# Performance work log

Hardware: AMD Instinct MI355X
Metric: run time of the kernel (lower is better)

## Reference

```python
import jax, jax.numpy as jnp
import numpy as np

B, N, DIM = 8, 16384, 256
DIM_HEAD, NUM_HEADS = 64, 8
D = DIM_HEAD * NUM_HEADS  # 512
SCALE = DIM_HEAD ** (-0.5)


def setup_inputs() -> dict:
    key = jax.random.key(0)
    ks = jax.random.split(key, 11)
    s = 0.02
    return {
        "x": jax.random.normal(ks[0], (B, N, DIM), dtype=jnp.float32),
        "Wq": jax.random.normal(ks[1], (DIM, D), dtype=jnp.float32) * s,
        "bq": jax.random.normal(ks[2], (D,), dtype=jnp.float32) * s,
        "Wk": jax.random.normal(ks[3], (DIM, D), dtype=jnp.float32) * s,
        "bk": jax.random.normal(ks[4], (D,), dtype=jnp.float32) * s,
        "qw": jax.random.normal(ks[5], (D, 1), dtype=jnp.float32),  # query_weight parameter
        "Wp": jax.random.normal(ks[6], (D, D), dtype=jnp.float32) * s,
        "bp": jax.random.normal(ks[7], (D,), dtype=jnp.float32) * s,
        "Wo": jax.random.normal(ks[8], (D, DIM_HEAD), dtype=jnp.float32) * s,
        "bo": jax.random.normal(ks[9], (DIM_HEAD,), dtype=jnp.float32) * s,
    }


def reference(x, Wq, bq, Wk, bk, qw, Wp, bp, Wo, bo):
    # query, key: [B, N, D]
    query = jnp.einsum("bnc,cd->bnd", x, Wq) + bq
    key = jnp.einsum("bnc,cd->bnd", x, Wk) + bk
    # per-token scalar score: [B, N, 1]
    score = (query @ qw) * SCALE
    # global attention context: sum over sequence axis -> [B, 1, D]
    attn_weight = jnp.sum(score * query, axis=1, keepdims=True)
    # broadcast (repeat over N), gate keys, project, residual add of query
    out = jnp.einsum("bnd,de->bne", attn_weight * key, Wp) + bp + query
    # output projection D -> dim_head: [B, N, DIM_HEAD]
    out = jnp.einsum("bnd,dh->bnh", out, Wo) + bo
    return out
```

## Files before the change

### kernel.cpp

```cpp
#include <hip/hip_runtime.h>
#include <hip/hip_bf16.h>


#define NN 16384
#define CC 256
#define DD 512
#define HH 64
#define SCALE_F 0.125f

#define OFF_SX    0
#define OFF_TSUM  2048
#define OFF_WQQ   2056
#define OFF_BQQ   2312
#define OFF_WPWO  2320
#define OFF_WQWO  35088
#define OFF_CBIAS 51472
#define OFF_BEFF  51536
#define OFF_WEFFT 52048

typedef unsigned short ushort_t;
typedef __attribute__((ext_vector_type(8))) short short8;
typedef __attribute__((ext_vector_type(4))) float floatx4;

__device__ __forceinline__ unsigned short f2bf(float f) {
    __hip_bfloat16 h = __float2bfloat16(f);
    return __builtin_bit_cast(unsigned short, h);
}

__global__ __launch_bounds__(256) void k_prep(
    const float* __restrict__ Wq, const float* __restrict__ bq,
    const float* __restrict__ qw, const float* __restrict__ Wp,
    const float* __restrict__ bp, const float* __restrict__ Wo,
    const float* __restrict__ bo, float* __restrict__ ws)
{
    __shared__ float lds[4096];
    const int tid = threadIdx.x;
    const int bid = blockIdx.x;

    if (bid < 64) {
        const int d0 = bid * 8;
        for (int i = tid; i < 4096; i += 256) lds[i] = Wp[d0 * 512 + i];
        __syncthreads();
        for (int o = tid; o < 512; o += 256) {
            const int dl = o >> 6, h = o & 63;
            float acc = 0.f;
            for (int e = 0; e < 512; ++e) acc += lds[dl * 512 + e] * Wo[e * 64 + h];
            ws[OFF_WPWO + (d0 + dl) * 64 + h] = acc;
        }
    } else if (bid == 64) {
        for (int i = tid; i < 512; i += 256) lds[i] = qw[i];
        __syncthreads();
        {
            const float* wr = Wq + tid * 512;
            float acc = 0.f;
            for (int d = 0; d < 512; ++d) acc += wr[d] * lds[d];
            ws[OFF_WQQ + tid] = acc;
        }
        if (tid == 0) {
            float s = 0.f;
            for (int d = 0; d < 512; ++d) s += bq[d] * lds[d];
            ws[OFF_BQQ] = s;
        }
        for (int i = tid; i < 2056; i += 256) ws[OFF_SX + i] = 0.f;
    } else if (bid == 65) {
        if (tid < 64) {
            float acc = bo[tid];
            for (int d = 0; d < 512; ++d) acc += (bq[d] + bp[d]) * Wo[d * 64 + tid];
            ws[OFF_CBIAS + tid] = acc;
        }
    } else {
        const int c0 = (bid - 66) * 8;
        for (int i = tid; i < 4096; i += 256) lds[i] = Wq[c0 * 512 + i];
        __syncthreads();
        for (int o = tid; o < 512; o += 256) {
            const int cl = o >> 6, h = o & 63;
            float acc = 0.f;
            for (int d = 0; d < 512; ++d) acc += lds[cl * 512 + d] * Wo[d * 64 + h];
            ws[OFF_WQWO + (c0 + cl) * 64 + h] = acc;
        }
    }
}

__global__ __launch_bounds__(256) void k_phase1(
    const float* __restrict__ x, float* __restrict__ ws)
{
    const int b = blockIdx.y;
    const int tid = threadIdx.x;
    const int lane = tid & 63;
    const int wave = tid >> 6;

    __shared__ float lacc[256];
    __shared__ float ltsum;
    lacc[tid] = 0.f;
    if (tid == 0) ltsum = 0.f;
    const floatx4 wv = *(const floatx4*)(ws + OFF_WQQ + lane * 4);
    const float bqq = ws[OFF_BQQ];
    __syncthreads();

    const int row0 = blockIdx.x * 128 + wave * 32;
    const float* xb = x + (size_t)b * NN * CC;

    float a0 = 0.f, a1 = 0.f, a2 = 0.f, a3 = 0.f, ts = 0.f;
    for (int i = 0; i < 32; ++i) {
        const floatx4 xv = *(const floatx4*)(xb + (size_t)(row0 + i) * CC + lane * 4);
        float p = xv[0] * wv[0] + xv[1] * wv[1] + xv[2] * wv[2] + xv[3] * wv[3];
        p += __shfl_xor(p, 32);
        p += __shfl_xor(p, 16);
        p += __shfl_xor(p, 8);
        p += __shfl_xor(p, 4);
        p += __shfl_xor(p, 2);
        p += __shfl_xor(p, 1);
        const float t = SCALE_F * (p + bqq);
        a0 += t * xv[0]; a1 += t * xv[1]; a2 += t * xv[2]; a3 += t * xv[3];
        ts += t;
    }
    atomicAdd(&lacc[lane * 4 + 0], a0);
    atomicAdd(&lacc[lane * 4 + 1], a1);
    atomicAdd(&lacc[lane * 4 + 2], a2);
    atomicAdd(&lacc[lane * 4 + 3], a3);
    if (lane == 0) atomicAdd(&ltsum, ts);
    __syncthreads();
    atomicAdd(&ws[OFF_SX + b * 256 + tid], lacc[tid]);
    if (tid == 0) atomicAdd(&ws[OFF_TSUM + b], ltsum);
}

__global__ __launch_bounds__(256) void k_weff(
    const float* __restrict__ Wq, const float* __restrict__ bq,
    const float* __restrict__ Wk, const float* __restrict__ bk,
    float* __restrict__ ws)
{
    const int b = blockIdx.y;
    const int c0 = blockIdx.x * 32;
    const int tid = threadIdx.x;

    __shared__ float lsx[256];
    __shared__ float law[512];
    __shared__ float lts;
    __shared__ float wpT[128 * 64];
    lsx[tid] = ws[OFF_SX + b * 256 + tid];
    if (tid == 0) lts = ws[OFF_TSUM + b];
    __syncthreads();
    const float tsum = lts;

    for (int d = tid; d < 512; d += 256) {
        float acc = tsum * bq[d];
        for (int c = 0; c < 256; ++c) acc += lsx[c] * Wq[c * 512 + d];
        law[d] = acc;
    }
    __syncthreads();

    const int c = c0 + (tid >> 3);
    const int hb = (tid & 7) * 8;
    float acc[8];
#pragma unroll
    for (int j = 0; j < 8; ++j) acc[j] = ws[OFF_WQWO + c * 64 + hb + j];

    for (int t4 = 0; t4 < 4; ++t4) {
        const int d0 = t4 * 128;
        for (int i = tid; i < 8192; i += 256) wpT[i] = ws[OFF_WPWO + d0 * 64 + i];
        __syncthreads();
        for (int dl = 0; dl < 128; ++dl) {
            const float g = Wk[c * 512 + d0 + dl] * law[d0 + dl];
            const floatx4 p0 = *(const floatx4*)(wpT + dl * 64 + hb);
            const floatx4 p1 = *(const floatx4*)(wpT + dl * 64 + hb + 4);
            acc[0] += g * p0[0]; acc[1] += g * p0[1];
            acc[2] += g * p0[2]; acc[3] += g * p0[3];
            acc[4] += g * p1[0]; acc[5] += g * p1[1];
            acc[6] += g * p1[2]; acc[7] += g * p1[3];
        }
        __syncthreads();
    }

    ushort_t* wt = (ushort_t*)(ws + OFF_WEFFT) + (size_t)b * (HH * CC);
#pragma unroll
    for (int j = 0; j < 8; ++j)
        wt[(size_t)(hb + j) * CC + c] = f2bf(acc[j]);

    if (blockIdx.x == 0 && tid < 64) {
        float a = ws[OFF_CBIAS + tid];
        for (int d = 0; d < 512; ++d)
            a += bk[d] * law[d] * ws[OFF_WPWO + d * 64 + tid];
        ws[OFF_BEFF + b * 64 + tid] = a;
    }
}

__global__ __launch_bounds__(256) void k_out(
    const float* __restrict__ x, const float* __restrict__ ws,
    float* __restrict__ out)
{
    const int b = blockIdx.y;
    const int tid = threadIdx.x;
    const int lane = tid & 63;
    const int wave = tid >> 6;
    const int quad = lane >> 4;
    const int l15 = lane & 15;
    const int row0 = blockIdx.x * 64 + wave * 16;

    __shared__ __align__(16) ushort_t lwt[64 * 264];
    const ushort_t* wt = (const ushort_t*)(ws + OFF_WEFFT) + (size_t)b * (HH * CC);
    for (int o = tid; o < 2048; o += 256) {
        const int h = o >> 5, seg = o & 31;
        *(short8*)(lwt + h * 264 + seg * 8) = *(const short8*)(wt + h * 256 + seg * 8);
    }

    const float* xr = x + ((size_t)b * NN + row0 + l15) * CC + quad * 8;
    short8 afrag[8];
#pragma unroll
    for (int kk = 0; kk < 8; ++kk) {
        const floatx4 u0 = *(const floatx4*)(xr + kk * 32);
        const floatx4 u1 = *(const floatx4*)(xr + kk * 32 + 4);
        short8 t;
        t[0] = (short)f2bf(u0[0]); t[1] = (short)f2bf(u0[1]);
        t[2] = (short)f2bf(u0[2]); t[3] = (short)f2bf(u0[3]);
        t[4] = (short)f2bf(u1[0]); t[5] = (short)f2bf(u1[1]);
        t[6] = (short)f2bf(u1[2]); t[7] = (short)f2bf(u1[3]);
        afrag[kk] = t;
    }
    __syncthreads();

    floatx4 acc[4];
#pragma unroll
    for (int ht = 0; ht < 4; ++ht)
#pragma unroll
        for (int r = 0; r < 4; ++r) acc[ht][r] = 0.f;

#pragma unroll
    for (int kk = 0; kk < 8; ++kk)
#pragma unroll
        for (int ht = 0; ht < 4; ++ht) {
            const short8 bf =
                *(const short8*)(lwt + (ht * 16 + l15) * 264 + quad * 8 + kk * 32);
            acc[ht] = __builtin_amdgcn_mfma_f32_16x16x32_bf16(
                afrag[kk], bf, acc[ht], 0, 0, 0);
        }

    const float* beff = ws + OFF_BEFF + b * 64;
#pragma unroll
    for (int ht = 0; ht < 4; ++ht) {
        const int h = ht * 16 + l15;
        const float bias = beff[h];
#pragma unroll
        for (int r = 0; r < 4; ++r) {
            const int row = row0 + quad * 4 + r;
            out[((size_t)b * NN + row) * HH + h] = acc[ht][r] + bias;
        }
    }
}

extern "C" void kernel_launch(void* const* d_in, const int* in_sizes, int n_in,
                              void* d_out, int out_size, void* d_ws, size_t ws_size,
                              hipStream_t stream) {
    const float* x  = (const float*)d_in[0];
    const float* Wq = (const float*)d_in[1];
    const float* bq = (const float*)d_in[2];
    const float* Wk = (const float*)d_in[3];
    const float* bk = (const float*)d_in[4];
    const float* qw = (const float*)d_in[5];
    const float* Wp = (const float*)d_in[6];
    const float* bp = (const float*)d_in[7];
    const float* Wo = (const float*)d_in[8];
    const float* bo = (const float*)d_in[9];
    float* ws = (float*)d_ws;
    float* out = (float*)d_out;

    hipLaunchKernelGGL(k_prep,   dim3(98),      dim3(256), 0, stream,
                       Wq, bq, qw, Wp, bp, Wo, bo, ws);
    hipLaunchKernelGGL(k_phase1, dim3(128, 8),  dim3(256), 0, stream, x, ws);
    hipLaunchKernelGGL(k_weff,   dim3(8, 8),    dim3(256), 0, stream,
                       Wq, bq, Wk, bk, ws);
    hipLaunchKernelGGL(k_out,    dim3(256, 8),  dim3(256), 0, stream, x, ws, out);
}
```

Before: 328.1 us.

## Fuse four kernels into one cooperative persistent kernel with grid syncs

Merges the prep, reduction, weight-fold and output kernels into a single cooperative launch of 1024 blocks, separated by grid-wide barriers, and falls back to four launches if the cooperative launch fails. The aim is to cut the launch gaps between small dependent kernels. It also reworks the phase-1 reduction so each lane holds 16 floats and reduces over fewer shuffles, and has each output block process two row tiles so the bf16 weight tile staged in LDS is reused. The risks are grid.sync overhead, lower occupancy from launch_bounds(256,4), and phase C running on only 64 blocks while the rest of the grid waits.

New measurement: 1.201 ms. 3.66x slower.

```diff
diff --git a/kernel.cpp b/kernel.cpp
--- a/kernel.cpp
+++ b/kernel.cpp
@@ -1,5 +1,6 @@
 #include <hip/hip_runtime.h>
 #include <hip/hip_bf16.h>
+#include <hip/hip_cooperative_groups.h>
 
 
 #define NN 16384
@@ -7,6 +8,8 @@
 #define DD 512
 #define HH 64
 #define SCALE_F 0.125f
+#define GRID_BLKS 1024
+#define SMEM_BYTES 33792
 
 #define OFF_SX    0
 #define OFF_TSUM  2048
@@ -27,224 +30,328 @@
     return __builtin_bit_cast(unsigned short, h);
 }
 
-__global__ __launch_bounds__(256) void k_prep(
+__device__ __forceinline__ void phaseA(
+    const float* __restrict__ Wq, const float* __restrict__ bq,
+    const float* __restrict__ qw, const float* __restrict__ Wp,
+    const float* __restrict__ bp, const float* __restrict__ Wo,
+    const float* __restrict__ bo, float* __restrict__ ws,
+    unsigned char* smem)
+{
+    const int tid = threadIdx.x;
+    for (int vb = blockIdx.x; vb < 195; vb += gridDim.x) {
+        if (vb < 128) {
+            float* lds = (float*)smem;
+            const int d0 = vb * 4;
+            for (int i = tid; i < 2048; i += 256) lds[i] = Wp[d0 * 512 + i];
+            __syncthreads();
+            const int dl = tid >> 6, h = tid & 63;
+            float acc = 0.f;
+            for (int e = 0; e < 512; ++e)
+                acc = fmaf(lds[dl * 512 + e], Wo[e * 64 + h], acc);
+            ws[OFF_WPWO + (d0 + dl) * 64 + h] = acc;
+        } else if (vb < 192) {
+            float* lds = (float*)smem;
+            const int c0 = (vb - 128) * 4;
+            for (int i = tid; i < 2048; i += 256) lds[i] = Wq[c0 * 512 + i];
+            __syncthreads();
+            const int cl = tid >> 6, h = tid & 63;
+            float acc = 0.f;
+            for (int e = 0; e < 512; ++e)
+                acc = fmaf(lds[cl * 512 + e], Wo[e * 64 + h], acc);
+            ws[OFF_WQWO + (c0 + cl) * 64 + h] = acc;
+        } else if (vb == 192) {
+            float* lds = (float*)smem;
+            float* lb  = (float*)(smem + 2048);
+            for (int i = tid; i < 512; i += 256) lds[i] = qw[i];
+            if (tid == 0) *lb = 0.f;
+            __syncthreads();
+            const float* wr = Wq + tid * 512;
+            float acc = 0.f;
+            for (int d = 0; d < 512; ++d) acc = fmaf(wr[d], lds[d], acc);
+            ws[OFF_WQQ + tid] = acc;
+            float pb = fmaf(bq[tid], lds[tid], bq[tid + 256] * lds[tid + 256]);
+#pragma unroll
+            for (int m = 1; m < 64; m <<= 1) pb += __shfl_xor(pb, m);
+            if ((tid & 63) == 0) atomicAdd(lb, pb);
+            __syncthreads();
+            if (tid == 0) ws[OFF_BQQ] = *lb;
+        } else if (vb == 193) {
+            if (tid < 64) {
+                float acc = bo[tid];
+                for (int d = 0; d < 512; ++d)
+                    acc = fmaf(bq[d] + bp[d], Wo[d * 64 + tid], acc);
+                ws[OFF_CBIAS + tid] = acc;
+            }
+        } else {
+            for (int i = tid; i < 2056; i += 256) ws[OFF_SX + i] = 0.f;
+        }
+        __syncthreads();
+    }
+}
+
+__device__ __forceinline__ void phaseB(
+    const float* __restrict__ x, float* __restrict__ ws, unsigned char* smem)
+{
+    const int tid  = threadIdx.x;
+    const int lane = tid & 63;
+    const int wave = tid >> 6;
+    const int quad = lane >> 4;
+    const int l15  = lane & 15;
+    float* lacc  = (float*)smem;
+    float* ltsum = (float*)(smem + 1024);
+
+    floatx4 wv[4];
+#pragma unroll
+    for (int j = 0; j < 4; ++j)
+        wv[j] = *(const floatx4*)(ws + OFF_WQQ + j * 64 + l15 * 4);
+    const float bqq = ws[OFF_BQQ];
+
+    for (int vb = blockIdx.x; vb < 1024; vb += gridDim.x) {
+        const int b = vb >> 7;
+        const int rbase = (vb & 127) * 128;
+        lacc[tid] = 0.f;
+        if (tid == 0) *ltsum = 0.f;
+        __syncthreads();
+
+        const float* xb = x + (size_t)b * NN * CC;
+        const int r0 = rbase + wave * 32 + quad;
+        floatx4 accs[4];
+#pragma unroll
+        for (int j = 0; j < 4; ++j)
+#pragma unroll
+            for (int k = 0; k < 4; ++k) accs[j][k] = 0.f;
+        float ts = 0.f;
+
+#pragma unroll 2
+        for (int it = 0; it < 8; ++it) {
+            const float* xr = xb + (size_t)(r0 + it * 4) * CC + l15 * 4;
+            const floatx4 x0 = *(const floatx4*)(xr);
+            const floatx4 x1 = *(const floatx4*)(xr + 64);
+            const floatx4 x2 = *(const floatx4*)(xr + 128);
+            const floatx4 x3 = *(const floatx4*)(xr + 192);
+            float p = 0.f;
+#pragma unroll
+            for (int k = 0; k < 4; ++k) {
+                p = fmaf(x0[k], wv[0][k], p);
+                p = fmaf(x1[k], wv[1][k], p);
+                p = fmaf(x2[k], wv[2][k], p);
+                p = fmaf(x3[k], wv[3][k], p);
+            }
+            p += __shfl_xor(p, 1);
+            p += __shfl_xor(p, 2);
+            p += __shfl_xor(p, 4);
+            p += __shfl_xor(p, 8);
+            const float t = SCALE_F * (p + bqq);
+            ts += t;
+#pragma unroll
+            for (int k = 0; k < 4; ++k) {
+                accs[0][k] = fmaf(t, x0[k], accs[0][k]);
+                accs[1][k] = fmaf(t, x1[k], accs[1][k]);
+                accs[2][k] = fmaf(t, x2[k], accs[2][k]);
+                accs[3][k] = fmaf(t, x3[k], accs[3][k]);
+            }
+        }
+
+#pragma unroll
+        for (int j = 0; j < 4; ++j)
+#pragma unroll
+            for (int k = 0; k < 4; ++k) {
+                float v = accs[j][k];
+                v += __shfl_xor(v, 16);
+                v += __shfl_xor(v, 32);
+                if (quad == 0) atomicAdd(&lacc[j * 64 + l15 * 4 + k], v);
+            }
+        if (l15 == 0) atomicAdd(ltsum, ts);
+        __syncthreads();
+        atomicAdd(&ws[OFF_SX + b * 256 + tid], lacc[tid]);
+        if (tid == 0) atomicAdd(&ws[OFF_TSUM + b], *ltsum);
+        __syncthreads();
+    }
+}
+
+__device__ __forceinline__ void phaseC(
+    const float* __restrict__ Wq, const float* __restrict__ bq,
+    const float* __restrict__ Wk, const float* __restrict__ bk,
+    float* __restrict__ ws, unsigned char* smem)
+{
+    const int tid = threadIdx.x;
+    for (int vb = blockIdx.x; vb < 64; vb += gridDim.x) {
+        const int b = vb >> 3;
+        const int c0 = (vb & 7) * 32;
+        float* lsx = (float*)smem;
+        float* law = (float*)(smem + 1024);
+        float* lts = (float*)(smem + 3072);
+        float* wpT = (float*)(smem + 3088);
+
+        lsx[tid] = ws[OFF_SX + b * 256 + tid];
+        if (tid == 0) *lts = ws[OFF_TSUM + b];
+        __syncthreads();
+        const float tsum = *lts;
+
+        for (int d = tid; d < 512; d += 256) {
+            float acc = tsum * bq[d];
+            for (int c = 0; c < 256; ++c) acc = fmaf(lsx[c], Wq[c * 512 + d], acc);
+            law[d] = acc;
+        }
+        __syncthreads();
+
+        const int c = c0 + (tid >> 3);
+        const int hb = (tid & 7) * 8;
+        float acc[8];
+#pragma unroll
+        for (int j = 0; j < 8; ++j) acc[j] = ws[OFF_WQWO + c * 64 + hb + j];
+
+        for (int t8 = 0; t8 < 8; ++t8) {
+            const int d0 = t8 * 64;
+            for (int i = tid; i < 4096; i += 256) wpT[i] = ws[OFF_WPWO + d0 * 64 + i];
+            __syncthreads();
+            for (int dl = 0; dl < 64; ++dl) {
+                const float g = Wk[c * 512 + d0 + dl] * law[d0 + dl];
+                const floatx4 p0 = *(const floatx4*)(wpT + dl * 64 + hb);
+                const floatx4 p1 = *(const floatx4*)(wpT + dl * 64 + hb + 4);
+                acc[0] = fmaf(g, p0[0], acc[0]); acc[1] = fmaf(g, p0[1], acc[1]);
+                acc[2] = fmaf(g, p0[2], acc[2]); acc[3] = fmaf(g, p0[3], acc[3]);
+                acc[4] = fmaf(g, p1[0], acc[4]); acc[5] = fmaf(g, p1[1], acc[5]);
+                acc[6] = fmaf(g, p1[2], acc[6]); acc[7] = fmaf(g, p1[3], acc[7]);
+            }
+            __syncthreads();
+        }
+
+        ushort_t* wt = (ushort_t*)(ws + OFF_WEFFT) + (size_t)b * (HH * CC);
+#pragma unroll
+        for (int j = 0; j < 8; ++j)
+            wt[(size_t)(hb + j) * CC + c] = f2bf(acc[j]);
+
+        if ((vb & 7) == 0 && tid < 64) {
+            float a = ws[OFF_CBIAS + tid];
+            for (int d = 0; d < 512; ++d)
+                a = fmaf(bk[d] * law[d], ws[OFF_WPWO + d * 64 + tid], a);
+            ws[OFF_BEFF + b * 64 + tid] = a;
+        }
+        __syncthreads();
+    }
+}
+
+__device__ __forceinline__ void phaseD(
+    const float* __restrict__ x, const float* __restrict__ ws,
+    float* __restrict__ out, unsigned char* smem)
+{
+    const int tid  = threadIdx.x;
+    const int lane = tid & 63;
+    const int wave = tid >> 6;
+    const int quad = lane >> 4;
+    const int l15  = lane & 15;
+    ushort_t* lwt = (ushort_t*)smem;
+
+    for (int vb = blockIdx.x; vb < 1024; vb += gridDim.x) {
+        const int b = vb >> 7;
+        const int rt0 = vb & 127;
+        const ushort_t* wt = (const ushort_t*)(ws + OFF_WEFFT) + (size_t)b * (HH * CC);
+        for (int o = tid; o < 2048; o += 256) {
+            const int h = o >> 5, seg = o & 31;
+            *(short8*)(lwt + h * 264 + seg * 8) = *(const short8*)(wt + h * 256 + seg * 8);
+        }
+        __syncthreads();
+
+        const float* beff = ws + OFF_BEFF + b * 64;
+        float bias[4];
+#pragma unroll
+        for (int ht = 0; ht < 4; ++ht) bias[ht] = beff[ht * 16 + l15];
+
+#pragma unroll
+        for (int s = 0; s < 2; ++s) {
+            const int row0 = (rt0 + s * 128) * 64 + wave * 16;
+            const float* xr = x + ((size_t)b * NN + row0 + l15) * CC + quad * 8;
+            short8 afrag[8];
+#pragma unroll
+            for (int kk = 0; kk < 8; ++kk) {
+                const floatx4 u0 = *(const floatx4*)(xr + kk * 32);
+                const floatx4 u1 = *(const floatx4*)(xr + kk * 32 + 4);
+                short8 t;
+                t[0] = (short)f2bf(u0[0]); t[1] = (short)f2bf(u0[1]);
+                t[2] = (short)f2bf(u0[2]); t[3] = (short)f2bf(u0[3]);
+                t[4] = (short)f2bf(u1[0]); t[5] = (short)f2bf(u1[1]);
+                t[6] = (short)f2bf(u1[2]); t[7] = (short)f2bf(u1[3]);
+                afrag[kk] = t;
+            }
+            floatx4 acc[4];
+#pragma unroll
+            for (int ht = 0; ht < 4; ++ht)
+#pragma unroll
+                for (int r = 0; r < 4; ++r) acc[ht][r] = 0.f;
+
+#pragma unroll
+            for (int kk = 0; kk < 8; ++kk)
+#pragma unroll
+                for (int ht = 0; ht < 4; ++ht) {
+                    const short8 bf =
+                        *(const short8*)(lwt + (ht * 16 + l15) * 264 + quad * 8 + kk * 32);
+                    acc[ht] = __builtin_amdgcn_mfma_f32_16x16x32_bf16(
+                        afrag[kk], bf, acc[ht], 0, 0, 0);
+                }
+
+#pragma unroll
+            for (int ht = 0; ht < 4; ++ht) {
+                const int h = ht * 16 + l15;
+#pragma unroll
+                for (int r = 0; r < 4; ++r) {
+                    const int row = row0 + quad * 4 + r;
+                    out[((size_t)b * NN + row) * HH + h] = acc[ht][r] + bias[ht];
+                }
+            }
+        }
+        __syncthreads();
+    }
+}
+
+__global__ __launch_bounds__(256, 4) void k_fused(
+    const float* __restrict__ x,  const float* __restrict__ Wq,
+    const float* __restrict__ bq, const float* __restrict__ Wk,
+    const float* __restrict__ bk, const float* __restrict__ qw,
+    const float* __restrict__ Wp, const float* __restrict__ bp,
+    const float* __restrict__ Wo, const float* __restrict__ bo,
+    float* __restrict__ ws, float* __restrict__ out)
+{
+    __shared__ __align__(16) unsigned char smem[SMEM_BYTES];
+    cooperative_groups::grid_group grid = cooperative_groups::this_grid();
+    phaseA(Wq, bq, qw, Wp, bp, Wo, bo, ws, smem);
+    grid.sync();
+    phaseB(x, ws, smem);
+    grid.sync();
+    phaseC(Wq, bq, Wk, bk, ws, smem);
+    grid.sync();
+    phaseD(x, ws, out, smem);
+}
+
+__global__ __launch_bounds__(256, 4) void k_phA(
     const float* __restrict__ Wq, const float* __restrict__ bq,
     const float* __restrict__ qw, const float* __restrict__ Wp,
     const float* __restrict__ bp, const float* __restrict__ Wo,
     const float* __restrict__ bo, float* __restrict__ ws)
 {
-    __shared__ float lds[4096];
-    const int tid = threadIdx.x;
-    const int bid = blockIdx.x;
-
-    if (bid < 64) {
-        const int d0 = bid * 8;
-        for (int i = tid; i < 4096; i += 256) lds[i] = Wp[d0 * 512 + i];
-        __syncthreads();
-        for (int o = tid; o < 512; o += 256) {
-            const int dl = o >> 6, h = o & 63;
-            float acc = 0.f;
-            for (int e = 0; e < 512; ++e) acc += lds[dl * 512 + e] * Wo[e * 64 + h];
-            ws[OFF_WPWO + (d0 + dl) * 64 + h] = acc;
-        }
-    } else if (bid == 64) {
-        for (int i = tid; i < 512; i += 256) lds[i] = qw[i];
-        __syncthreads();
-        {
-            const float* wr = Wq + tid * 512;
-            float acc = 0.f;
-            for (int d = 0; d < 512; ++d) acc += wr[d] * lds[d];
-            ws[OFF_WQQ + tid] = acc;
-        }
-        if (tid == 0) {
-            float s = 0.f;
-            for (int d = 0; d < 512; ++d) s += bq[d] * lds[d];
-            ws[OFF_BQQ] = s;
-        }
-        for (int i = tid; i < 2056; i += 256) ws[OFF_SX + i] = 0.f;
-    } else if (bid == 65) {
-        if (tid < 64) {
-            float acc = bo[tid];
-            for (int d = 0; d < 512; ++d) acc += (bq[d] + bp[d]) * Wo[d * 64 + tid];
-            ws[OFF_CBIAS + tid] = acc;
-        }
-    } else {
-        const int c0 = (bid - 66) * 8;
-        for (int i = tid; i < 4096; i += 256) lds[i] = Wq[c0 * 512 + i];
-        __syncthreads();
-        for (int o = tid; o < 512; o += 256) {
-            const int cl = o >> 6, h = o & 63;
-            float acc = 0.f;
-            for (int d = 0; d < 512; ++d) acc += lds[cl * 512 + d] * Wo[d * 64 + h];
-            ws[OFF_WQWO + (c0 + cl) * 64 + h] = acc;
-        }
-    }
-}
-
-__global__ __launch_bounds__(256) void k_phase1(
+    __shared__ __align__(16) unsigned char smem[SMEM_BYTES];
+    phaseA(Wq, bq, qw, Wp, bp, Wo, bo, ws, smem);
+}
+__global__ __launch_bounds__(256, 4) void k_phB(
     const float* __restrict__ x, float* __restrict__ ws)
 {
-    const int b = blockIdx.y;
-    const int tid = threadIdx.x;
-    const int lane = tid & 63;
-    const int wave = tid >> 6;
-
-    __shared__ float lacc[256];
-    __shared__ float ltsum;
-    lacc[tid] = 0.f;
-    if (tid == 0) ltsum = 0.f;
-    const floatx4 wv = *(const floatx4*)(ws + OFF_WQQ + lane * 4);
-    const float bqq = ws[OFF_BQQ];
-    __syncthreads();
-
-    const int row0 = blockIdx.x * 128 + wave * 32;
-    const float* xb = x + (size_t)b * NN * CC;
-
-    float a0 = 0.f, a1 = 0.f, a2 = 0.f, a3 = 0.f, ts = 0.f;
-    for (int i = 0; i < 32; ++i) {
-        const floatx4 xv = *(const floatx4*)(xb + (size_t)(row0 + i) * CC + lane * 4);
-        float p = xv[0] * wv[0] + xv[1] * wv[1] + xv[2] * wv[2] + xv[3] * wv[3];
-        p += __shfl_xor(p, 32);
-        p += __shfl_xor(p, 16);
-        p += __shfl_xor(p, 8);
-        p += __shfl_xor(p, 4);
-        p += __shfl_xor(p, 2);
-        p += __shfl_xor(p, 1);
-        const float t = SCALE_F * (p + bqq);
-        a0 += t * xv[0]; a1 += t * xv[1]; a2 += t * xv[2]; a3 += t * xv[3];
-        ts += t;
-    }
-    atomicAdd(&lacc[lane * 4 + 0], a0);
-    atomicAdd(&lacc[lane * 4 + 1], a1);
-    atomicAdd(&lacc[lane * 4 + 2], a2);
-    atomicAdd(&lacc[lane * 4 + 3], a3);
-    if (lane == 0) atomicAdd(&ltsum, ts);
-    __syncthreads();
-    atomicAdd(&ws[OFF_SX + b * 256 + tid], lacc[tid]);
-    if (tid == 0) atomicAdd(&ws[OFF_TSUM + b], ltsum);
-}
-
-__global__ __launch_bounds__(256) void k_weff(
+    __shared__ __align__(16) unsigned char smem[SMEM_BYTES];
+    phaseB(x, ws, smem);
+}
+__global__ __launch_bounds__(256, 4) void k_phC(
     const float* __restrict__ Wq, const float* __restrict__ bq,
     const float* __restrict__ Wk, const float* __restrict__ bk,
     float* __restrict__ ws)
 {
-    const int b = blockIdx.y;
-    const int c0 = blockIdx.x * 32;
-    const int tid = threadIdx.x;
-
-    __shared__ float lsx[256];
-    __shared__ float law[512];
-    __shared__ float lts;
-    __shared__ float wpT[128 * 64];
-    lsx[tid] = ws[OFF_SX + b * 256 + tid];
-    if (tid == 0) lts = ws[OFF_TSUM + b];
-    __syncthreads();
-    const float tsum = lts;
-
-    for (int d = tid; d < 512; d += 256) {
-        float acc = tsum * bq[d];
-        for (int c = 0; c < 256; ++c) acc += lsx[c] * Wq[c * 512 + d];
-        law[d] = acc;
-    }
-    __syncthreads();
-
-    const int c = c0 + (tid >> 3);
-    const int hb = (tid & 7) * 8;
-    float acc[8];
-#pragma unroll
-    for (int j = 0; j < 8; ++j) acc[j] = ws[OFF_WQWO + c * 64 + hb + j];
-
-    for (int t4 = 0; t4 < 4; ++t4) {
-        const int d0 = t4 * 128;
-        for (int i = tid; i < 8192; i += 256) wpT[i] = ws[OFF_WPWO + d0 * 64 + i];
-        __syncthreads();
-        for (int dl = 0; dl < 128; ++dl) {
-            const float g = Wk[c * 512 + d0 + dl] * law[d0 + dl];
-            const floatx4 p0 = *(const floatx4*)(wpT + dl * 64 + hb);
-            const floatx4 p1 = *(const floatx4*)(wpT + dl * 64 + hb + 4);
-            acc[0] += g * p0[0]; acc[1] += g * p0[1];
-            acc[2] += g * p0[2]; acc[3] += g * p0[3];
-            acc[4] += g * p1[0]; acc[5] += g * p1[1];
-            acc[6] += g * p1[2]; acc[7] += g * p1[3];
-        }
-        __syncthreads();
-    }
-
-    ushort_t* wt = (ushort_t*)(ws + OFF_WEFFT) + (size_t)b * (HH * CC);
-#pragma unroll
-    for (int j = 0; j < 8; ++j)
-        wt[(size_t)(hb + j) * CC + c] = f2bf(acc[j]);
-
-    if (blockIdx.x == 0 && tid < 64) {
-        float a = ws[OFF_CBIAS + tid];
-        for (int d = 0; d < 512; ++d)
-            a += bk[d] * law[d] * ws[OFF_WPWO + d * 64 + tid];
-        ws[OFF_BEFF + b * 64 + tid] = a;
-    }
-}
-
-__global__ __launch_bounds__(256) void k_out(
+    __shared__ __align__(16) unsigned char smem[SMEM_BYTES];
+    phaseC(Wq, bq, Wk, bk, ws, smem);
+}
+__global__ __launch_bounds__(256, 4) void k_phD(
     const float* __restrict__ x, const float* __restrict__ ws,
     float* __restrict__ out)
 {
-    const int b = blockIdx.y;
-    const int tid = threadIdx.x;
-    const int lane = tid & 63;
-    const int wave = tid >> 6;
-    const int quad = lane >> 4;
-    const int l15 = lane & 15;
-    const int row0 = blockIdx.x * 64 + wave * 16;
-
-    __shared__ __align__(16) ushort_t lwt[64 * 264];
-    const ushort_t* wt = (const ushort_t*)(ws + OFF_WEFFT) + (size_t)b * (HH * CC);
-    for (int o = tid; o < 2048; o += 256) {
-        const int h = o >> 5, seg = o & 31;
-        *(short8*)(lwt + h * 264 + seg * 8) = *(const short8*)(wt + h * 256 + seg * 8);
-    }
-
-    const float* xr = x + ((size_t)b * NN + row0 + l15) * CC + quad * 8;
-    short8 afrag[8];
-#pragma unroll
-    for (int kk = 0; kk < 8; ++kk) {
-        const floatx4 u0 = *(const floatx4*)(xr + kk * 32);
-        const floatx4 u1 = *(const floatx4*)(xr + kk * 32 + 4);
-        short8 t;
-        t[0] = (short)f2bf(u0[0]); t[1] = (short)f2bf(u0[1]);
-        t[2] = (short)f2bf(u0[2]); t[3] = (short)f2bf(u0[3]);
-        t[4] = (short)f2bf(u1[0]); t[5] = (short)f2bf(u1[1]);
-        t[6] = (short)f2bf(u1[2]); t[7] = (short)f2bf(u1[3]);
-        afrag[kk] = t;
-    }
-    __syncthreads();
-
-    floatx4 acc[4];
-#pragma unroll
-    for (int ht = 0; ht < 4; ++ht)
-#pragma unroll
-        for (int r = 0; r < 4; ++r) acc[ht][r] = 0.f;
-
-#pragma unroll
-    for (int kk = 0; kk < 8; ++kk)
-#pragma unroll
-        for (int ht = 0; ht < 4; ++ht) {
-            const short8 bf =
-                *(const short8*)(lwt + (ht * 16 + l15) * 264 + quad * 8 + kk * 32);
-            acc[ht] = __builtin_amdgcn_mfma_f32_16x16x32_bf16(
-                afrag[kk], bf, acc[ht], 0, 0, 0);
-        }
-
-    const float* beff = ws + OFF_BEFF + b * 64;
-#pragma unroll
-    for (int ht = 0; ht < 4; ++ht) {
-        const int h = ht * 16 + l15;
-        const float bias = beff[h];
-#pragma unroll
-        for (int r = 0; r < 4; ++r) {
-            const int row = row0 + quad * 4 + r;
-            out[((size_t)b * NN + row) * HH + h] = acc[ht][r] + bias;
-        }
-    }
+    __shared__ __align__(16) unsigned char smem[SMEM_BYTES];
+    phaseD(x, ws, out, smem);
 }
 
 extern "C" void kernel_launch(void* const* d_in, const int* in_sizes, int n_in,
@@ -260,13 +367,21 @@
     const float* bp = (const float*)d_in[7];
     const float* Wo = (const float*)d_in[8];
     const float* bo = (const float*)d_in[9];
-    float* ws = (float*)d_ws;
+    float* ws  = (float*)d_ws;
     float* out = (float*)d_out;
 
-    hipLaunchKernelGGL(k_prep,   dim3(98),      dim3(256), 0, stream,
-                       Wq, bq, qw, Wp, bp, Wo, bo, ws);
-    hipLaunchKernelGGL(k_phase1, dim3(128, 8),  dim3(256), 0, stream, x, ws);
-    hipLaunchKernelGGL(k_weff,   dim3(8, 8),    dim3(256), 0, stream,
-                       Wq, bq, Wk, bk, ws);
-    hipLaunchKernelGGL(k_out,    dim3(256, 8),  dim3(256), 0, stream, x, ws, out);
-}
+    void* args[12] = {
+        (void*)&x,  (void*)&Wq, (void*)&bq, (void*)&Wk, (void*)&bk, (void*)&qw,
+        (void*)&Wp, (void*)&bp, (void*)&Wo, (void*)&bo, (void*)&ws, (void*)&out};
+
+    hipError_t err = hipLaunchCooperativeKernel(
+        (void*)k_fused, dim3(GRID_BLKS), dim3(256), args, 0, stream);
+    if (err != hipSuccess) {
+        hipLaunchKernelGGL(k_phA, dim3(195),  dim3(256), 0, stream,
+                           Wq, bq, qw, Wp, bp, Wo, bo, ws);
+        hipLaunchKernelGGL(k_phB, dim3(1024), dim3(256), 0, stream, x, ws);
+        hipLaunchKernelGGL(k_phC, dim3(64),   dim3(256), 0, stream,
+                           Wq, bq, Wk, bk, ws);
+        hipLaunchKernelGGL(k_phD, dim3(1024), dim3(256), 0, stream, x, ws, out);
+    }
+}
```
